# Kernel tuning notes

Measured on AMD Instinct MI355X. Metric: run time of the kernel, lower is better.

The kernel has to match this reference:

```python
import jax, jax.numpy as jnp
import numpy as np

EMBED_DIM = 1024
NUM_HEADS = 16
HEAD_DIM = EMBED_DIM // NUM_HEADS
MLP_SIZE = 4096
LN_EPS = 1e-5


def setup_inputs() -> dict:
    key = jax.random.key(0)
    ks = jax.random.split(key, 12)
    d, f = EMBED_DIM, MLP_SIZE
    s = lambda fan_in: 1.0 / np.sqrt(fan_in)
    return {
        "x": jax.random.normal(ks[0], (2, 2048, d), dtype=jnp.float32),
        "ln1_g": jnp.ones((d,), jnp.float32),
        "ln1_b": jnp.zeros((d,), jnp.float32),
        "ln2_g": jnp.ones((d,), jnp.float32),
        "ln2_b": jnp.zeros((d,), jnp.float32),
        "w_qkv": jax.random.uniform(ks[1], (d, 3 * d), jnp.float32, -s(d), s(d)),
        "b_qkv": jax.random.uniform(ks[2], (3 * d,), jnp.float32, -s(d), s(d)),
        "w_proj": jax.random.uniform(ks[3], (d, d), jnp.float32, -s(d), s(d)),
        "b_proj": jax.random.uniform(ks[4], (d,), jnp.float32, -s(d), s(d)),
        "w_fc1": jax.random.uniform(ks[5], (d, f), jnp.float32, -s(d), s(d)),
        "b_fc1": jax.random.uniform(ks[6], (f,), jnp.float32, -s(d), s(d)),
        "w_fc2": jax.random.uniform(ks[7], (f, d), jnp.float32, -s(f), s(f)),
        "b_fc2": jax.random.uniform(ks[8], (d,), jnp.float32, -s(f), s(f)),
    }


def _layernorm(x, g, b):
    mu = jnp.mean(x, axis=-1, keepdims=True)
    var = jnp.mean(jnp.square(x - mu), axis=-1, keepdims=True)
    return (x - mu) * jax.lax.rsqrt(var + LN_EPS) * g + b


def reference(x, ln1_g, ln1_b, ln2_g, ln2_b, w_qkv, b_qkv, w_proj, b_proj,
              w_fc1, b_fc1, w_fc2, b_fc2):
    B, N, C = x.shape
    H, D = NUM_HEADS, HEAD_DIM
    scale = D ** -0.5

    # --- attention sub-block (pre-LN) ---
    h = _layernorm(x, ln1_g, ln1_b)
    qkv = h @ w_qkv + b_qkv                      # [B,N,3C]
    qkv = qkv.reshape(B, N, 3, H, D)
    q, k, v = (jnp.moveaxis(qkv, 2, 0)[i].transpose(0, 2, 1, 3) for i in range(3))  # each [B,H,N,D]
    attn = jnp.einsum("bhnd,bhmd->bhnm", q, k) * scale
    attn = jax.nn.softmax(attn, axis=-1)
    o = jnp.einsum("bhnm,bhmd->bhnd", attn, v)   # [B,H,N,D]
    o = o.transpose(0, 2, 1, 3).reshape(B, N, C)
    x = x + (o @ w_proj + b_proj)

    # --- MLP sub-block (pre-LN) ---
    h = _layernorm(x, ln2_g, ln2_b)
    h = jax.nn.gelu(h @ w_fc1 + b_fc1, approximate=False)
    x = x + (h @ w_fc2 + b_fc2)
    return x
```

## Files before the change

kernel.cpp:

```cpp
#include <hip/hip_runtime.h>
#include <hip/hip_bf16.h>

typedef __attribute__((ext_vector_type(8))) __bf16 bf16x8;
typedef __attribute__((ext_vector_type(4))) float f32x4;
typedef unsigned short u16;

__device__ __forceinline__ float bf2f(u16 u) {
    unsigned int i = ((unsigned int)u) << 16;
    return __builtin_bit_cast(float, i);
}
__device__ __forceinline__ u16 f2bf_u16(float f) {
    __hip_bfloat16 h = __float2bfloat16(f);
    return *(u16*)&h;
}
__device__ __forceinline__ float gelu_f(float v) {
    return 0.5f * v * (1.0f + erff(v * 0.70710678118654752440f));
}
__device__ __forceinline__ bool is_f32(const unsigned* p) { return *p == 0x3F800000u; }
__device__ __forceinline__ bf16x8 ld_bf8_b64x2(const u16* p) {
    uint2 lo = *(const uint2*)p;
    uint2 hi = *(const uint2*)(p + 4);
    uint4 v = make_uint4(lo.x, lo.y, hi.x, hi.y);
    return __builtin_bit_cast(bf16x8, v);
}
__device__ __forceinline__ void async16(const void* g, void* l) {
    __builtin_amdgcn_global_load_lds(
        (const __attribute__((address_space(1))) void*)g,
        (__attribute__((address_space(3))) void*)l, 16, 0, 0);
}

__device__ __forceinline__ void conv8(const void* src, u16* dst, long off, bool f32in) {
    if (f32in) {
        const float* s = (const float*)src + off;
        float4 a = *(const float4*)s, b = *(const float4*)(s + 4);
        u16 o[8] = {f2bf_u16(a.x), f2bf_u16(a.y), f2bf_u16(a.z), f2bf_u16(a.w),
                    f2bf_u16(b.x), f2bf_u16(b.y), f2bf_u16(b.z), f2bf_u16(b.w)};
        *(uint4*)(dst + off) = *(const uint4*)o;
    } else {
        *(uint4*)(dst + off) = *(const uint4*)((const u16*)src + off);
    }
}

__global__ __launch_bounds__(256) void conv_bias(
        const void* __restrict__ bq, const void* __restrict__ bp,
        const void* __restrict__ b1, const void* __restrict__ b2,
        u16* dbq, u16* dbp, u16* db1, u16* db2,
        const unsigned* __restrict__ dtp) {
    long e = ((long)blockIdx.x * 256 + threadIdx.x) * 8;
    if (e >= 9216L) return;
    bool f = is_f32(dtp);
    if      (e < 3072L) conv8(bq, dbq, e, f);
    else if (e < 4096L) conv8(bp, dbp, e - 3072L, f);
    else if (e < 8192L) conv8(b1, db1, e - 4096L, f);
    else                conv8(b2, db2, e - 8192L, f);
}

__global__ __launch_bounds__(256) void conv_t(const void* __restrict__ src,
                                              u16* __restrict__ dst,
                                              int K, int N,
                                              const unsigned* __restrict__ dtp) {
    const bool f32in = is_f32(dtp);
    __shared__ u16 T[64 * 68];
    int k0 = blockIdx.y * 64, n0 = blockIdx.x * 64;
    int t = threadIdx.x;
    int kr = t >> 2, nc = (t & 3) * 16;

    u16 tmp[16];
    if (f32in) {
        const float* s = (const float*)src + (size_t)(k0 + kr) * N + n0 + nc;
        float4 a = *(const float4*)s;
        float4 b = *(const float4*)(s + 4);
        float4 c = *(const float4*)(s + 8);
        float4 d = *(const float4*)(s + 12);
        tmp[0]=f2bf_u16(a.x);  tmp[1]=f2bf_u16(a.y);  tmp[2]=f2bf_u16(a.z);  tmp[3]=f2bf_u16(a.w);
        tmp[4]=f2bf_u16(b.x);  tmp[5]=f2bf_u16(b.y);  tmp[6]=f2bf_u16(b.z);  tmp[7]=f2bf_u16(b.w);
        tmp[8]=f2bf_u16(c.x);  tmp[9]=f2bf_u16(c.y);  tmp[10]=f2bf_u16(c.z); tmp[11]=f2bf_u16(c.w);
        tmp[12]=f2bf_u16(d.x); tmp[13]=f2bf_u16(d.y); tmp[14]=f2bf_u16(d.z); tmp[15]=f2bf_u16(d.w);
    } else {
        const u16* s = (const u16*)src + (size_t)(k0 + kr) * N + n0 + nc;
        *(uint4*)&tmp[0] = *(const uint4*)s;
        *(uint4*)&tmp[8] = *(const uint4*)(s + 8);
    }
    u16* dl = &T[kr * 68 + nc];
    #pragma unroll
    for (int j = 0; j < 4; ++j)
        *(uint2*)(dl + 4 * j) = *(const uint2*)&tmp[4 * j];
    __syncthreads();

    int nr = t >> 2, kc = (t & 3) * 16;
    u16 o[16];
    #pragma unroll
    for (int i = 0; i < 16; ++i) o[i] = T[(kc + i) * 68 + nr];
    u16* dp = dst + (size_t)(n0 + nr) * K + k0 + kc;
    *(uint4*)dp       = *(const uint4*)&o[0];
    *(uint4*)(dp + 8) = *(const uint4*)&o[8];
}

__global__ __launch_bounds__(256) void vt_prep(const u16* __restrict__ qkv,
                                               unsigned* __restrict__ vtg) {
    __shared__ unsigned Vt[64 * 32];
    int bx = blockIdx.x;
    int b = bx >> 9, h = (bx >> 5) & 15, kt = bx & 31;
    int t = threadIdx.x;
    int va = t & 31, vdc = t >> 5;
    size_t vb = ((size_t)(b * 2048 + kt * 64 + 2 * va)) * 3072 + 2048 + h * 64 + vdc * 8;
    uint4 v0 = *(const uint4*)(qkv + vb);
    uint4 v1 = *(const uint4*)(qkv + vb + 3072);
    const u16* p0 = (const u16*)&v0;
    const u16* p1 = (const u16*)&v1;
    #pragma unroll
    for (int j = 0; j < 8; ++j)
        Vt[(vdc * 8 + j) * 32 + va] = (unsigned)p0[j] | ((unsigned)p1[j] << 16);
    __syncthreads();
    unsigned* dst = vtg + (size_t)bx * 2048 + t * 8;
    *(uint4*)dst       = *(const uint4*)&Vt[t * 8];
    *(uint4*)(dst + 4) = *(const uint4*)&Vt[t * 8 + 4];
}

__global__ __launch_bounds__(256) void ln_first(const void* __restrict__ xin,
                                                const void* __restrict__ g,
                                                const void* __restrict__ b,
                                                __hip_bfloat16* __restrict__ out,
                                                const unsigned* __restrict__ dtp) {
    const bool f32in = is_f32(dtp);
    int row = blockIdx.x, t = threadIdx.x;
    size_t base = (size_t)row * 1024 + 4 * t;
    float v[4];
    if (f32in) {
        float4 f = *(const float4*)((const float*)xin + base);
        v[0] = f.x; v[1] = f.y; v[2] = f.z; v[3] = f.w;
    } else {
        ushort4 u = *(const ushort4*)((const __hip_bfloat16*)xin + base);
        v[0] = bf2f(u.x); v[1] = bf2f(u.y); v[2] = bf2f(u.z); v[3] = bf2f(u.w);
    }
    float s = v[0] + v[1] + v[2] + v[3];
    float s2 = v[0]*v[0] + v[1]*v[1] + v[2]*v[2] + v[3]*v[3];
    #pragma unroll
    for (int off = 32; off > 0; off >>= 1) {
        s  += __shfl_down(s, off);
        s2 += __shfl_down(s2, off);
    }
    __shared__ float red[8];
    int wave = t >> 6, lane = t & 63;
    if (lane == 0) { red[wave] = s; red[4 + wave] = s2; }
    __syncthreads();
    float S  = red[0] + red[1] + red[2] + red[3];
    float S2 = red[4] + red[5] + red[6] + red[7];
    float mean = S * (1.0f / 1024.0f);
    float var  = S2 * (1.0f / 1024.0f) - mean * mean;
    float rstd = rsqrtf(var + 1e-5f);
    float gg[4], bb[4];
    if (f32in) {
        float4 fg = *(const float4*)((const float*)g + 4 * t);
        float4 fb = *(const float4*)((const float*)b + 4 * t);
        gg[0]=fg.x; gg[1]=fg.y; gg[2]=fg.z; gg[3]=fg.w;
        bb[0]=fb.x; bb[1]=fb.y; bb[2]=fb.z; bb[3]=fb.w;
    } else {
        ushort4 ug = *(const ushort4*)((const __hip_bfloat16*)g + 4 * t);
        ushort4 ub = *(const ushort4*)((const __hip_bfloat16*)b + 4 * t);
        gg[0]=bf2f(ug.x); gg[1]=bf2f(ug.y); gg[2]=bf2f(ug.z); gg[3]=bf2f(ug.w);
        bb[0]=bf2f(ub.x); bb[1]=bf2f(ub.y); bb[2]=bf2f(ub.z); bb[3]=bf2f(ub.w);
    }
    #pragma unroll
    for (int i = 0; i < 4; ++i)
        out[base + i] = __float2bfloat16((v[i] - mean) * rstd * gg[i] + bb[i]);
}

__global__ __launch_bounds__(256) void ln_mid(const float* __restrict__ x,
                                              const void* __restrict__ g,
                                              const void* __restrict__ b,
                                              __hip_bfloat16* __restrict__ out,
                                              const unsigned* __restrict__ dtp) {
    const bool f32in = is_f32(dtp);
    int row = blockIdx.x, t = threadIdx.x;
    size_t base = (size_t)row * 1024 + 4 * t;
    float4 f = *(const float4*)(x + base);
    float v[4] = {f.x, f.y, f.z, f.w};
    float s = v[0] + v[1] + v[2] + v[3];
    float s2 = v[0]*v[0] + v[1]*v[1] + v[2]*v[2] + v[3]*v[3];
    #pragma unroll
    for (int off = 32; off > 0; off >>= 1) {
        s  += __shfl_down(s, off);
        s2 += __shfl_down(s2, off);
    }
    __shared__ float red[8];
    int wave = t >> 6, lane = t & 63;
    if (lane == 0) { red[wave] = s; red[4 + wave] = s2; }
    __syncthreads();
    float S  = red[0] + red[1] + red[2] + red[3];
    float S2 = red[4] + red[5] + red[6] + red[7];
    float mean = S * (1.0f / 1024.0f);
    float var  = S2 * (1.0f / 1024.0f) - mean * mean;
    float rstd = rsqrtf(var + 1e-5f);
    float gg[4], bb[4];
    if (f32in) {
        float4 fg = *(const float4*)((const float*)g + 4 * t);
        float4 fb = *(const float4*)((const float*)b + 4 * t);
        gg[0]=fg.x; gg[1]=fg.y; gg[2]=fg.z; gg[3]=fg.w;
        bb[0]=fb.x; bb[1]=fb.y; bb[2]=fb.z; bb[3]=fb.w;
    } else {
        ushort4 ug = *(const ushort4*)((const __hip_bfloat16*)g + 4 * t);
        ushort4 ub = *(const ushort4*)((const __hip_bfloat16*)b + 4 * t);
        gg[0]=bf2f(ug.x); gg[1]=bf2f(ug.y); gg[2]=bf2f(ug.z); gg[3]=bf2f(ug.w);
        bb[0]=bf2f(ub.x); bb[1]=bf2f(ub.y); bb[2]=bf2f(ub.z); bb[3]=bf2f(ub.w);
    }
    #pragma unroll
    for (int i = 0; i < 4; ++i)
        out[base + i] = __float2bfloat16((v[i] - mean) * rstd * gg[i] + bb[i]);
}

template<int EPI, int BM, int BN>
__global__ __launch_bounds__(256, 2)
void gemm_bf16(const u16* __restrict__ A,
               const u16* __restrict__ BT,
               const u16* __restrict__ bias,
               const void* __restrict__ res,
               void* __restrict__ outp,
               int M, int N, int K,
               const unsigned* __restrict__ dtp) {
    constexpr int NI = BM / 32, NJ = BN / 32;
    constexpr int ASZ = BM * 32, BSZ = BN * 32;
    const bool f32in = is_f32(dtp);
    __shared__ __align__(16) u16 As[2 * ASZ];
    __shared__ __align__(16) u16 Bs[2 * BSZ];
    (void)M;

    int t = threadIdx.x;
    int w = t >> 6, lane = t & 63;
    int quad = lane >> 4, lq = lane & 15;
    int bm = blockIdx.y * BM, bn = blockIdx.x * BN;
    int wm = (w & 1) * (16 * NI), wn = (w >> 1) * (16 * NJ);

    int sr = lane >> 2, sc = (lane & 3) * 8;
    u16* aldst = &As[w * (BM * 8) + lane * 8];
    const u16* ag = A + (size_t)(bm + w * (BM / 4) + sr) * K + sc;
    u16* bldst = &Bs[w * (BN * 8) + lane * 8];
    const u16* bg = BT + (size_t)(bn + w * (BN / 4) + sr) * K + sc;

    f32x4 acc[NI][NJ];
    #pragma unroll
    for (int i = 0; i < NI; ++i)
        #pragma unroll
        for (int j = 0; j < NJ; ++j)
            #pragma unroll
            for (int r = 0; r < 4; ++r) acc[i][j][r] = 0.0f;

    async16(ag, aldst);
    if constexpr (BM == 128) async16(ag + (size_t)16 * K, aldst + 512);
    async16(bg, bldst);
    if constexpr (BN == 128) async16(bg + (size_t)16 * K, bldst + 512);

    const int nIter = K >> 5;
    for (int k = 0; k < nIter; ++k) {
        __syncthreads();
        int cur = k & 1;
        if (k + 1 < nIter) {
            int nxt = cur ^ 1;
            const u16* agn = ag + (size_t)(k + 1) * 32;
            async16(agn, aldst + nxt * ASZ);
            if constexpr (BM == 128) async16(agn + (size_t)16 * K, aldst + nxt * ASZ + 512);
            const u16* bgn = bg + (size_t)(k + 1) * 32;
            async16(bgn, bldst + nxt * BSZ);
            if constexpr (BN == 128) async16(bgn + (size_t)16 * K, bldst + nxt * BSZ + 512);
        }

        const u16* Ac = &As[cur * ASZ];
        const u16* Bc = &Bs[cur * BSZ];
        bf16x8 af[NI], bfr[NJ];
        #pragma unroll
        for (int i = 0; i < NI; ++i)
            af[i] = *(const bf16x8*)&Ac[(wm + 16 * i + lq) * 32 + quad * 8];
        #pragma unroll
        for (int j = 0; j < NJ; ++j)
            bfr[j] = *(const bf16x8*)&Bc[(wn + 16 * j + lq) * 32 + quad * 8];
        #pragma unroll
        for (int i = 0; i < NI; ++i)
            #pragma unroll
            for (int j = 0; j < NJ; ++j)
                acc[i][j] = __builtin_amdgcn_mfma_f32_16x16x32_bf16(af[i], bfr[j], acc[i][j], 0, 0, 0);
    }

    #pragma unroll
    for (int i = 0; i < NI; ++i) {
        #pragma unroll
        for (int j = 0; j < NJ; ++j) {
            #pragma unroll
            for (int r = 0; r < 4; ++r) {
                int row = bm + wm + 16 * i + quad * 4 + r;
                int col = bn + wn + 16 * j + lq;
                size_t idx = (size_t)row * N + col;
                float v = acc[i][j][r] + bf2f(bias[col]);
                if constexpr (EPI == 0) {
                    ((__hip_bfloat16*)outp)[idx] = __float2bfloat16(v);
                } else if constexpr (EPI == 1) {
                    v += f32in ? ((const float*)res)[idx]
                               : bf2f(((const u16*)res)[idx]);
                    ((float*)outp)[idx] = v;
                } else if constexpr (EPI == 2) {
                    ((__hip_bfloat16*)outp)[idx] = __float2bfloat16(gelu_f(v));
                } else {
                    v += ((const float*)res)[idx];
                    if (f32in) ((float*)outp)[idx] = v;
                    else       ((__hip_bfloat16*)outp)[idx] = __float2bfloat16(v);
                }
            }
        }
    }
}

__global__ __launch_bounds__(256, 4)
void attn_mfma(const __hip_bfloat16* __restrict__ qkv,
               const unsigned* __restrict__ vtg,
               __hip_bfloat16* __restrict__ o_out) {
    __shared__ __align__(16) u16 Ks[64 * 72];
    __shared__ __align__(16) unsigned Vt[64 * 36];
    __shared__ __align__(16) u16 Ps[64 * 68];

    int t = threadIdx.x;
    int lane = t & 63, w = t >> 6;
    int quad = lane >> 4, lq = lane & 15;
    int bx = blockIdx.x;
    int b  = bx >> 9, h = (bx >> 5) & 15, qt = bx & 31;
    size_t tok0 = (size_t)b * 2048;

    {
        int key = t >> 2, ld = (t & 3) * 16;
        size_t qb = (tok0 + (size_t)qt * 64 + key) * 3072 + h * 64 + ld;
        uint4 a0 = *(const uint4*)(qkv + qb);
        uint4 a1 = *(const uint4*)(qkv + qb + 8);
        const u16* s0 = (const u16*)&a0;
        const u16* s1 = (const u16*)&a1;
        u16 q16[16];
        #pragma unroll
        for (int j = 0; j < 8; ++j) {
            q16[j]     = f2bf_u16(bf2f(s0[j]) * 0.125f);
            q16[8 + j] = f2bf_u16(bf2f(s1[j]) * 0.125f);
        }
        u16* dst = &Ps[key * 68 + ld];
        #pragma unroll
        for (int j4 = 0; j4 < 4; ++j4)
            *(uint2*)(dst + 4 * j4) = *(const uint2*)&q16[4 * j4];
    }
    __syncthreads();
    bf16x8 qf0 = ld_bf8_b64x2(&Ps[(w * 16 + lq) * 68 + quad * 8]);
    bf16x8 qf1 = ld_bf8_b64x2(&Ps[(w * 16 + lq) * 68 + quad * 8 + 32]);

    f32x4 oacc[4];
    #pragma unroll
    for (int dt = 0; dt < 4; ++dt)
        #pragma unroll
        for (int r = 0; r < 4; ++r) oacc[dt][r] = 0.0f;
    float m_run = -1e30f, l_run = 0.0f;

    int skey = t >> 2, sld = (t & 3) * 16;
    int vrow = t >> 2, vcol = (t & 3) * 8;

    for (int kt = 0; kt < 32; ++kt) {
        __syncthreads();
        {
            size_t kb = (tok0 + (size_t)kt * 64 + skey) * 3072 + 1024 + h * 64 + sld;
            uint4 k0 = *(const uint4*)(qkv + kb);
            uint4 k1 = *(const uint4*)(qkv + kb + 8);
            *(uint4*)&Ks[skey * 72 + sld]     = k0;
            *(uint4*)&Ks[skey * 72 + sld + 8] = k1;
        }
        {
            const unsigned* vg = vtg + ((size_t)(b * 512 + h * 32 + kt)) * 2048 + t * 8;
            uint4 w0 = *(const uint4*)vg;
            uint4 w1 = *(const uint4*)(vg + 4);
            unsigned* vdst = &Vt[vrow * 36 + vcol];
            *(uint4*)vdst       = w0;
            *(uint4*)(vdst + 4) = w1;
        }
        __syncthreads();

        f32x4 sacc[4];
        #pragma unroll
        for (int j = 0; j < 4; ++j)
            #pragma unroll
            for (int r = 0; r < 4; ++r) sacc[j][r] = 0.0f;
        #pragma unroll
        for (int j = 0; j < 4; ++j) {
            const u16* kr = &Ks[(j * 16 + lq) * 72 + quad * 8];
            bf16x8 kf0 = *(const bf16x8*)kr;
            bf16x8 kf1 = *(const bf16x8*)(kr + 32);
            sacc[j] = __builtin_amdgcn_mfma_f32_16x16x32_bf16(kf0, qf0, sacc[j], 0, 0, 0);
            sacc[j] = __builtin_amdgcn_mfma_f32_16x16x32_bf16(kf1, qf1, sacc[j], 0, 0, 0);
        }

        float mx = sacc[0][0];
        #pragma unroll
        for (int j = 0; j < 4; ++j)
            #pragma unroll
            for (int r = 0; r < 4; ++r) mx = fmaxf(mx, sacc[j][r]);
        mx = fmaxf(mx, __shfl_xor(mx, 16));
        mx = fmaxf(mx, __shfl_xor(mx, 32));
        float mnew = fmaxf(m_run, mx);
        if (__any(mnew > m_run)) {
            float alpha = __expf(m_run - mnew);
            l_run *= alpha;
            #pragma unroll
            for (int dt = 0; dt < 4; ++dt)
                #pragma unroll
                for (int r = 0; r < 4; ++r) oacc[dt][r] *= alpha;
        }
        m_run = mnew;

        float ls = 0.0f;
        int prow = (w * 16 + lq) * 68;
        #pragma unroll
        for (int j = 0; j < 4; ++j) {
            float p0 = __expf(sacc[j][0] - mnew);
            float p1 = __expf(sacc[j][1] - mnew);
            float p2 = __expf(sacc[j][2] - mnew);
            float p3 = __expf(sacc[j][3] - mnew);
            ls += (p0 + p1) + (p2 + p3);
            u16 pk[4] = {f2bf_u16(p0), f2bf_u16(p1), f2bf_u16(p2), f2bf_u16(p3)};
            *(uint2*)&Ps[prow + quad * 4 + 16 * j] = *(const uint2*)pk;
        }
        ls += __shfl_xor(ls, 16);
        ls += __shfl_xor(ls, 32);
        l_run += ls;

        bf16x8 pf0 = ld_bf8_b64x2(&Ps[prow + quad * 8]);
        bf16x8 pf1 = ld_bf8_b64x2(&Ps[prow + quad * 8 + 32]);
        #pragma unroll
        for (int dt = 0; dt < 4; ++dt) {
            const unsigned* vr = &Vt[(dt * 16 + lq) * 36 + quad * 4];
            bf16x8 vf0 = __builtin_bit_cast(bf16x8, *(const uint4*)vr);
            bf16x8 vf1 = __builtin_bit_cast(bf16x8, *(const uint4*)(vr + 16));
            oacc[dt] = __builtin_amdgcn_mfma_f32_16x16x32_bf16(vf0, pf0, oacc[dt], 0, 0, 0);
            oacc[dt] = __builtin_amdgcn_mfma_f32_16x16x32_bf16(vf1, pf1, oacc[dt], 0, 0, 0);
        }
    }

    __syncthreads();
    u16* T = Ks;
    float inv = 1.0f / l_run;
    int trow = (w * 16 + lq) * 68;
    #pragma unroll
    for (int dt = 0; dt < 4; ++dt) {
        u16 pk[4] = {f2bf_u16(oacc[dt][0] * inv), f2bf_u16(oacc[dt][1] * inv),
                     f2bf_u16(oacc[dt][2] * inv), f2bf_u16(oacc[dt][3] * inv)};
        *(uint2*)&T[trow + quad * 4 + 16 * dt] = *(const uint2*)pk;
    }
    __syncthreads();
    {
        int q = t >> 2, dc = (t & 3) * 16;
        const u16* src = &T[q * 68 + dc];
        uint2 a0 = *(const uint2*)src;
        uint2 a1 = *(const uint2*)(src + 4);
        uint2 a2 = *(const uint2*)(src + 8);
        uint2 a3 = *(const uint2*)(src + 12);
        u16* op = (u16*)o_out + (tok0 + (size_t)qt * 64 + q) * 1024 + h * 64 + dc;
        *(uint4*)op       = make_uint4(a0.x, a0.y, a1.x, a1.y);
        *(uint4*)(op + 8) = make_uint4(a2.x, a2.y, a3.x, a3.y);
    }
}

extern "C" void kernel_launch(void* const* d_in, const int* in_sizes, int n_in,
                              void* d_out, int out_size, void* d_ws, size_t ws_size,
                              hipStream_t stream) {
    (void)in_sizes; (void)n_in; (void)out_size; (void)ws_size;
    const void* x      = d_in[0];
    const void* ln1_g  = d_in[1];
    const void* ln1_b  = d_in[2];
    const void* ln2_g  = d_in[3];
    const void* ln2_b  = d_in[4];
    const void* w_qkv  = d_in[5];
    const void* b_qkv  = d_in[6];
    const void* w_proj = d_in[7];
    const void* b_proj = d_in[8];
    const void* w_fc1  = d_in[9];
    const void* b_fc1  = d_in[10];
    const void* w_fc2  = d_in[11];
    const void* b_fc2  = d_in[12];
    const unsigned* probe = (const unsigned*)ln1_g;

    constexpr int Mtok = 4096;
    char* ws = (char*)d_ws;
    __hip_bfloat16* bufA = (__hip_bfloat16*)ws;
    __hip_bfloat16* qkvb = (__hip_bfloat16*)(ws + ((size_t)8 << 20));
    float*          x1   = (float*)(ws + ((size_t)8 << 20));
    u16*            w1T  = (u16*)(ws + ((size_t)24 << 20));
    u16*            wqT  = (u16*)(ws + ((size_t)32 << 20));
    u16*            wpT  = (u16*)(ws + ((size_t)38 << 20));
    unsigned*       vtg  = (unsigned*)(ws + ((size_t)40 << 20));
    __hip_bfloat16* g1   = (__hip_bfloat16*)(ws + ((size_t)32 << 20));
    u16*            w2T  = (u16*)ws;
    char* BZ = ws + ((size_t)64 << 20);
    u16* bqb = (u16*)BZ;
    u16* bpb = (u16*)(BZ + 8192);
    u16* b1b = (u16*)(BZ + 16384);
    u16* b2b = (u16*)(BZ + 24576);

    conv_bias<<<5, 256, 0, stream>>>(b_qkv, b_proj, b_fc1, b_fc2,
                                     bqb, bpb, b1b, b2b, probe);
    conv_t<<<dim3(3072 / 64, 1024 / 64), 256, 0, stream>>>(w_qkv, wqT, 1024, 3072, probe);
    conv_t<<<dim3(1024 / 64, 1024 / 64), 256, 0, stream>>>(w_proj, wpT, 1024, 1024, probe);
    ln_first<<<Mtok, 256, 0, stream>>>(x, ln1_g, ln1_b, bufA, probe);
    gemm_bf16<0, 128, 128><<<dim3(3072 / 128, Mtok / 128), 256, 0, stream>>>(
        (const u16*)bufA, wqT, bqb, nullptr, qkvb, Mtok, 3072, 1024, probe);
    vt_prep<<<1024, 256, 0, stream>>>((const u16*)qkvb, vtg);
    attn_mfma<<<1024, 256, 0, stream>>>(qkvb, vtg, bufA);
    conv_t<<<dim3(4096 / 64, 1024 / 64), 256, 0, stream>>>(w_fc1, w1T, 1024, 4096, probe);
    gemm_bf16<1, 64, 64><<<dim3(1024 / 64, Mtok / 64), 256, 0, stream>>>(
        (const u16*)bufA, wpT, bpb, x, x1, Mtok, 1024, 1024, probe);
    ln_mid<<<Mtok, 256, 0, stream>>>(x1, ln2_g, ln2_b, bufA, probe);
    gemm_bf16<2, 128, 128><<<dim3(4096 / 128, Mtok / 128), 256, 0, stream>>>(
        (const u16*)bufA, w1T, b1b, nullptr, g1, Mtok, 4096, 1024, probe);
    conv_t<<<dim3(1024 / 64, 4096 / 64), 256, 0, stream>>>(w_fc2, w2T, 4096, 1024, probe);
    gemm_bf16<3, 64, 64><<<dim3(1024 / 64, Mtok / 64), 256, 0, stream>>>(
        (const u16*)g1, w2T, b2b, x1, d_out, Mtok, 1024, 4096, probe);
}
```

Measured before the change: 396.6 us.

## Prefetch K/V tiles into registers, lazily rescale softmax, enlarge proj/fc2 GEMM tiles

The attention loop now issues global loads for the next K and V tile into registers right after the barrier, so the load latency overlaps with the current tile's MFMA and softmax work. Online-softmax rescaling is skipped unless the new row max exceeds the running max by more than 8, which avoids the rescale and running-max updates on most iterations but lets the exp arguments grow up to e^8 before correction. The proj and fc2 GEMMs switch from 64x64 to 128x64 tiles, which halves the grid and raises per-block reuse. Costs are extra registers for the prefetch and fewer blocks for the two smaller GEMMs.

After: 400.2 us. No clear change (+0.9%).

```diff
diff --git a/kernel.cpp b/kernel.cpp
--- a/kernel.cpp
+++ b/kernel.cpp
@@ -355,24 +355,32 @@
     int skey = t >> 2, sld = (t & 3) * 16;
     int vrow = t >> 2, vcol = (t & 3) * 8;
 
+    uint4 k0, k1, w0, w1;
+    {
+        size_t kb = (tok0 + (size_t)skey) * 3072 + 1024 + h * 64 + sld;
+        k0 = *(const uint4*)(qkv + kb);
+        k1 = *(const uint4*)(qkv + kb + 8);
+        const unsigned* vg = vtg + ((size_t)(b * 512 + h * 32)) * 2048 + t * 8;
+        w0 = *(const uint4*)vg;
+        w1 = *(const uint4*)(vg + 4);
+    }
+
     for (int kt = 0; kt < 32; ++kt) {
         __syncthreads();
-        {
-            size_t kb = (tok0 + (size_t)kt * 64 + skey) * 3072 + 1024 + h * 64 + sld;
-            uint4 k0 = *(const uint4*)(qkv + kb);
-            uint4 k1 = *(const uint4*)(qkv + kb + 8);
-            *(uint4*)&Ks[skey * 72 + sld]     = k0;
-            *(uint4*)&Ks[skey * 72 + sld + 8] = k1;
-        }
-        {
-            const unsigned* vg = vtg + ((size_t)(b * 512 + h * 32 + kt)) * 2048 + t * 8;
-            uint4 w0 = *(const uint4*)vg;
-            uint4 w1 = *(const uint4*)(vg + 4);
-            unsigned* vdst = &Vt[vrow * 36 + vcol];
-            *(uint4*)vdst       = w0;
-            *(uint4*)(vdst + 4) = w1;
-        }
+        *(uint4*)&Ks[skey * 72 + sld]     = k0;
+        *(uint4*)&Ks[skey * 72 + sld + 8] = k1;
+        unsigned* vdst = &Vt[vrow * 36 + vcol];
+        *(uint4*)vdst       = w0;
+        *(uint4*)(vdst + 4) = w1;
         __syncthreads();
+        if (kt + 1 < 32) {
+            size_t kb = (tok0 + (size_t)(kt + 1) * 64 + skey) * 3072 + 1024 + h * 64 + sld;
+            k0 = *(const uint4*)(qkv + kb);
+            k1 = *(const uint4*)(qkv + kb + 8);
+            const unsigned* vg = vtg + ((size_t)(b * 512 + h * 32 + kt + 1)) * 2048 + t * 8;
+            w0 = *(const uint4*)vg;
+            w1 = *(const uint4*)(vg + 4);
+        }
 
         f32x4 sacc[4];
         #pragma unroll
@@ -395,25 +403,25 @@
             for (int r = 0; r < 4; ++r) mx = fmaxf(mx, sacc[j][r]);
         mx = fmaxf(mx, __shfl_xor(mx, 16));
         mx = fmaxf(mx, __shfl_xor(mx, 32));
-        float mnew = fmaxf(m_run, mx);
-        if (__any(mnew > m_run)) {
+        if (!__all(mx <= m_run + 8.0f)) {
+            float mnew = fmaxf(m_run, mx);
             float alpha = __expf(m_run - mnew);
             l_run *= alpha;
             #pragma unroll
             for (int dt = 0; dt < 4; ++dt)
                 #pragma unroll
                 for (int r = 0; r < 4; ++r) oacc[dt][r] *= alpha;
-        }
-        m_run = mnew;
+            m_run = mnew;
+        }
 
         float ls = 0.0f;
         int prow = (w * 16 + lq) * 68;
         #pragma unroll
         for (int j = 0; j < 4; ++j) {
-            float p0 = __expf(sacc[j][0] - mnew);
-            float p1 = __expf(sacc[j][1] - mnew);
-            float p2 = __expf(sacc[j][2] - mnew);
-            float p3 = __expf(sacc[j][3] - mnew);
+            float p0 = __expf(sacc[j][0] - m_run);
+            float p1 = __expf(sacc[j][1] - m_run);
+            float p2 = __expf(sacc[j][2] - m_run);
+            float p3 = __expf(sacc[j][3] - m_run);
             ls += (p0 + p1) + (p2 + p3);
             u16 pk[4] = {f2bf_u16(p0), f2bf_u16(p1), f2bf_u16(p2), f2bf_u16(p3)};
             *(uint2*)&Ps[prow + quad * 4 + 16 * j] = *(const uint2*)pk;
@@ -504,12 +512,12 @@
     vt_prep<<<1024, 256, 0, stream>>>((const u16*)qkvb, vtg);
     attn_mfma<<<1024, 256, 0, stream>>>(qkvb, vtg, bufA);
     conv_t<<<dim3(4096 / 64, 1024 / 64), 256, 0, stream>>>(w_fc1, w1T, 1024, 4096, probe);
-    gemm_bf16<1, 64, 64><<<dim3(1024 / 64, Mtok / 64), 256, 0, stream>>>(
+    gemm_bf16<1, 128, 64><<<dim3(1024 / 64, Mtok / 128), 256, 0, stream>>>(
         (const u16*)bufA, wpT, bpb, x, x1, Mtok, 1024, 1024, probe);
     ln_mid<<<Mtok, 256, 0, stream>>>(x1, ln2_g, ln2_b, bufA, probe);
     gemm_bf16<2, 128, 128><<<dim3(4096 / 128, Mtok / 128), 256, 0, stream>>>(
         (const u16*)bufA, w1T, b1b, nullptr, g1, Mtok, 4096, 1024, probe);
     conv_t<<<dim3(1024 / 64, 4096 / 64), 256, 0, stream>>>(w_fc2, w2T, 4096, 1024, probe);
-    gemm_bf16<3, 64, 64><<<dim3(1024 / 64, Mtok / 64), 256, 0, stream>>>(
+    gemm_bf16<3, 128, 64><<<dim3(1024 / 64, Mtok / 128), 256, 0, stream>>>(
         (const u16*)g1, w2T, b2b, x1, d_out, Mtok, 1024, 4096, probe);
 }
```
